# Performance work log

Measured on AMD Instinct MI355X. Metric: run time of the kernel, lower is better.

Reference implementation:

```python
import jax, jax.numpy as jnp
import numpy as np

# Dims from LiftSplatShootGPN defaults
B, N, D, FH, FW, C = 8, 6, 41, 8, 22, 64
OGFH, OGFW = 128, 352
DX = jnp.array([0.5, 0.5, 20.0], dtype=jnp.float32)        # gen_dx_bx
BX = jnp.array([-49.75, -49.75, 0.0], dtype=jnp.float32)
NX = (200, 200, 1)


def _frustum():
    # D x fH x fW x 3, matches create_frustum
    ds = jnp.broadcast_to(jnp.arange(4.0, 45.0, 1.0, dtype=jnp.float32).reshape(D, 1, 1), (D, FH, FW))
    xs = jnp.broadcast_to(jnp.linspace(0.0, OGFW - 1.0, FW, dtype=jnp.float32).reshape(1, 1, FW), (D, FH, FW))
    ys = jnp.broadcast_to(jnp.linspace(0.0, OGFH - 1.0, FH, dtype=jnp.float32).reshape(1, FH, 1), (D, FH, FW))
    return jnp.stack((xs, ys, ds), -1)


def setup_inputs() -> dict:
    key = jax.random.key(0)
    k1, k2, k3, k4, k5, k6 = jax.random.split(key, 6)
    eye = jnp.eye(3, dtype=jnp.float32)
    x_feats = jax.random.normal(k1, (B, N, D, FH, FW, C), dtype=jnp.float32)
    # well-conditioned camera extrinsics / intrinsics
    rots = eye + 0.1 * jax.random.normal(k2, (B, N, 3, 3), dtype=jnp.float32)
    trans = 2.0 * jax.random.normal(k3, (B, N, 3), dtype=jnp.float32)
    intr_base = jnp.array([[278.0, 0.0, 176.0], [0.0, 278.0, 64.0], [0.0, 0.0, 1.0]], dtype=jnp.float32)
    intrins = intr_base + 0.5 * jax.random.normal(k4, (B, N, 3, 3), dtype=jnp.float32) * jnp.array([[1, 0, 1], [0, 1, 1], [0, 0, 0]], dtype=jnp.float32)
    post_rots = eye + 0.01 * jax.random.normal(k5, (B, N, 3, 3), dtype=jnp.float32)
    post_trans = 0.5 * jax.random.normal(k6, (B, N, 3), dtype=jnp.float32)
    return {"x_feats": x_feats, "rots": rots, "trans": trans, "intrins": intrins,
            "post_rots": post_rots, "post_trans": post_trans}


def _forward(x_feats, rots, trans, intrins, post_rots, post_trans):
    frustum = _frustum()  # [D,FH,FW,3]
    # get_geometry: undo image-space augmentation
    pts = frustum[None, None] - post_trans[:, :, None, None, None, :]            # [B,N,D,H,W,3]
    inv_pr = jnp.linalg.inv(post_rots)                                           # [B,N,3,3]
    pts = jnp.einsum('bnij,bndhwj->bndhwi', inv_pr, pts)
    # unproject: (u*d, v*d, d)
    pts = jnp.concatenate((pts[..., :2] * pts[..., 2:3], pts[..., 2:3]), axis=-1)
    combine = jnp.einsum('bnij,bnjk->bnik', rots, jnp.linalg.inv(intrins))
    geom = jnp.einsum('bnij,bndhwj->bndhwi', combine, pts) + trans[:, :, None, None, None, :]

    # voxel_pooling
    Nprime = B * N * D * FH * FW
    x = x_feats.reshape(Nprime, C)
    # torch .long() truncates toward zero -> astype(int32) matches
    g = ((geom - (BX - DX / 2.0)) / DX).reshape(Nprime, 3).astype(jnp.int32)
    bix = jnp.repeat(jnp.arange(B, dtype=jnp.int32), Nprime // B)
    kept = ((g[:, 0] >= 0) & (g[:, 0] < NX[0]) &
            (g[:, 1] >= 0) & (g[:, 1] < NX[1]) &
            (g[:, 2] >= 0) & (g[:, 2] < NX[2]))
    # QuickCumsum computes per-voxel segment sums; scatter-add of all kept points
    # into the dense grid yields identical values without the sort.
    flat = ((bix * NX[2] + g[:, 2]) * NX[0] + g[:, 0]) * NX[1] + g[:, 1]
    flat = jnp.where(kept, flat, 0)
    xm = jnp.where(kept[:, None], x, jnp.zeros((), x.dtype))
    grid = jnp.zeros((B * NX[2] * NX[0] * NX[1], C), dtype=x.dtype).at[flat].add(xm)
    # final: [B, C, nz, nx0, nx1] -> cat over nz (nz=1) -> [B, C, 200, 200]
    grid = grid.reshape(B, NX[2], NX[0], NX[1], C)
    final = jnp.transpose(grid, (0, 1, 4, 2, 3)).reshape(B, NX[2] * C, NX[0], NX[1])
    return final


def reference(x_feats, rots, trans, intrins, post_rots, post_trans):
    return _forward(x_feats, rots, trans, intrins, post_rots, post_trans)
```

## Files before the change

kernel.cpp:

```cpp
#include <hip/hip_runtime.h>

#define B_   8
#define N_   6
#define D_   41
#define FH_  8
#define FW_  22
#define C_   64
#define NPRIME (B_*N_*D_*FH_*FW_)
#define NBLK_PTS 1353
#define PTS_PER_CAM (D_*FH_*FW_)
#define NX0  200
#define NX1  200
#define G1H  2
#define NB2  (B_ * NX0 * G1H)
#define OUTSZ (B_*C_*NX0*NX1)
#define RROWS 4
#define NGRP  50
#define KINT  25
#define NCH   4

__device__ void lapack_inv3_f32(const float Ain[9], float Aout[9]) {
    #pragma clang fp contract(off)
    float a[9];
    for (int r = 0; r < 3; ++r)
        for (int c = 0; c < 3; ++c)
            a[c*3 + r] = Ain[r*3 + c];
    int ipiv[3];
    for (int j = 0; j < 3; ++j) {
        int p = j;
        float amax = fabsf(a[j*3 + j]);
        for (int i = j + 1; i < 3; ++i) {
            float v = fabsf(a[j*3 + i]);
            if (v > amax) { amax = v; p = i; }
        }
        ipiv[j] = p;
        if (p != j)
            for (int c = 0; c < 3; ++c) { float t = a[c*3+j]; a[c*3+j] = a[c*3+p]; a[c*3+p] = t; }
        float d = 1.0f / a[j*3 + j];
        for (int i = j + 1; i < 3; ++i) a[j*3 + i] = a[j*3 + i] * d;
        for (int jj = j + 1; jj < 3; ++jj) {
            float temp = -a[jj*3 + j];
            for (int ii = j + 1; ii < 3; ++ii)
                a[jj*3 + ii] = a[jj*3 + ii] + a[j*3 + ii] * temp;
        }
    }
    for (int j = 0; j < 3; ++j) {
        float ajj_inv = 1.0f / a[j*3 + j];
        a[j*3 + j] = ajj_inv;
        float AJJ = -ajj_inv;
        for (int jj = 0; jj < j; ++jj) {
            float temp = a[j*3 + jj];
            for (int i = 0; i < jj; ++i)
                a[j*3 + i] = a[j*3 + i] + temp * a[jj*3 + i];
            a[j*3 + jj] = a[j*3 + jj] * a[jj*3 + jj];
        }
        for (int i = 0; i < j; ++i) a[j*3 + i] = a[j*3 + i] * AJJ;
    }
    float work[3];
    for (int j = 2; j >= 0; --j) {
        for (int i = j + 1; i < 3; ++i) { work[i] = a[j*3 + i]; a[j*3 + i] = 0.0f; }
        for (int jj = j + 1; jj < 3; ++jj) {
            float temp = -work[jj];
            for (int i = 0; i < 3; ++i)
                a[j*3 + i] = a[j*3 + i] + temp * a[jj*3 + i];
        }
    }
    for (int j = 2; j >= 0; --j) {
        int p = ipiv[j];
        if (p != j)
            for (int i = 0; i < 3; ++i) { float t = a[j*3+i]; a[j*3+i] = a[p*3+i]; a[p*3+i] = t; }
    }
    for (int r = 0; r < 3; ++r)
        for (int c = 0; c < 3; ++c)
            Aout[r*3 + c] = a[c*3 + r];
}

__global__ void prep_kernel(const float* __restrict__ rots,
                            const float* __restrict__ trans,
                            const float* __restrict__ intrins,
                            const float* __restrict__ post_rots,
                            const float* __restrict__ post_trans,
                            float* __restrict__ mats,
                            int* __restrict__ counts) {
    #pragma clang fp contract(off)
    int t = threadIdx.x;
    for (int i = t; i < NB2; i += 256) counts[i] = 0;
    if (t >= B_ * N_) return;
    float pr[9], ipr[9], K[9], iK[9];
    for (int i = 0; i < 9; ++i) { pr[i] = post_rots[t*9 + i]; K[i] = intrins[t*9 + i]; }
    lapack_inv3_f32(pr, ipr);
    lapack_inv3_f32(K, iK);
    float* m = mats + t * 24;
    for (int i = 0; i < 9; ++i) m[i] = ipr[i];
    for (int i = 0; i < 3; ++i)
        for (int k = 0; k < 3; ++k) {
            float s = rots[t*9 + i*3 + 0] * iK[0*3 + k];
            s = s + rots[t*9 + i*3 + 1] * iK[1*3 + k];
            s = s + rots[t*9 + i*3 + 2] * iK[2*3 + k];
            m[9 + i*3 + k] = s;
        }
    for (int i = 0; i < 3; ++i) {
        m[18 + i] = post_trans[t*3 + i];
        m[21 + i] = trans[t*3 + i];
    }
}

__global__ void __launch_bounds__(256) geom_kernel(
        const float* __restrict__ mats,
        unsigned int* __restrict__ pcode,
        int* __restrict__ counts) {
    #pragma clang fp contract(off)
    __shared__ unsigned int hist[NB2];
    int t = threadIdx.x;
    int p = blockIdx.x * 256 + t;
    for (int i = t; i < NB2; i += 256) hist[i] = 0u;
    __syncthreads();

    int w  = p % FW_;
    int h  = (p / FW_) % FH_;
    int d  = (p / (FW_ * FH_)) % D_;
    int bn = p / PTS_PER_CAM;
    int b  = bn / N_;

    const float* m = mats + bn * 24;

    float xs = (w == FW_ - 1) ? 351.0f : (float)((double)w * (351.0 / 21.0));
    float ys = (h == FH_ - 1) ? 127.0f : (float)((double)h * (127.0 / 7.0));
    float ds = 4.0f + (float)d;

    float px = xs - m[18], py = ys - m[19], pz = ds - m[20];
    float qx = m[0]*px;  qx = qx + m[1]*py;  qx = qx + m[2]*pz;
    float qy = m[3]*px;  qy = qy + m[4]*py;  qy = qy + m[5]*pz;
    float qz = m[6]*px;  qz = qz + m[7]*py;  qz = qz + m[8]*pz;

    float ux = qx * qz, uy = qy * qz, uz = qz;

    float gx = m[9]*ux;   gx = gx + m[10]*uy;  gx = gx + m[11]*uz;  gx = gx + m[21];
    float gy = m[12]*ux;  gy = gy + m[13]*uy;  gy = gy + m[14]*uz;  gy = gy + m[22];
    float gz = m[15]*ux;  gz = gz + m[16]*uy;  gz = gz + m[17]*uz;  gz = gz + m[23];

    float cx = (gx - (-50.0f)) / 0.5f;
    float cy = (gy - (-50.0f)) / 0.5f;
    float cz = (gz - (-10.0f)) / 20.0f;
    int g0 = (int)cx;
    int g1 = (int)cy;
    int g2 = (int)cz;

    bool kept = (g0 >= 0) && (g0 < NX0) && (g1 >= 0) && (g1 < NX1) && (g2 == 0);
    if (kept) {
        int g1h = g1 / 100;
        int r   = g1 - g1h * 100;
        int bk  = (b * NX0 + g0) * G1H + g1h;
        pcode[p] = ((unsigned int)bk << 7) | (unsigned int)r;
        atomicAdd(&hist[bk], 1u);
    } else {
        pcode[p] = 0xFFFFFFFFu;
    }
    __syncthreads();
    for (int i = t; i < NB2; i += 256) {
        unsigned int hv = hist[i];
        if (hv) atomicAdd(&counts[i], (int)hv);
    }
}

__global__ void scan_kernel(const int* __restrict__ counts,
                            int* __restrict__ offsets,
                            int* __restrict__ cursor) {
    __shared__ int ts[128];
    int t = threadIdx.x;
    const int PER = NB2 / 128;
    int base = t * PER;
    int mysum = 0;
    for (int j = 0; j < PER; ++j) mysum += counts[base + j];
    ts[t] = mysum;
    __syncthreads();
    for (int off = 1; off < 128; off <<= 1) {
        int v = (t >= off) ? ts[t - off] : 0;
        __syncthreads();
        ts[t] += v;
        __syncthreads();
    }
    int run = (t > 0) ? ts[t - 1] : 0;
    for (int j = 0; j < PER; ++j) {
        offsets[base + j] = run;
        cursor[base + j]  = run;
        run += counts[base + j];
    }
    if (t == 127) offsets[NB2] = run;
}

__global__ void __launch_bounds__(256) place_kernel(
        const unsigned int* __restrict__ pcode,
        int* __restrict__ cursor,
        unsigned int* __restrict__ entries) {
    __shared__ int cnt[NB2];
    int t = threadIdx.x;
    int p = blockIdx.x * 256 + t;
    for (int i = t; i < NB2; i += 256) cnt[i] = 0;
    __syncthreads();
    unsigned int code = pcode[p];
    bool kept = (code != 0xFFFFFFFFu);
    int bk = (int)(code >> 7);
    int lr = 0;
    if (kept) lr = atomicAdd(&cnt[bk], 1);
    __syncthreads();
    for (int i = t; i < NB2; i += 256) {
        int c = cnt[i];
        if (c) cnt[i] = atomicAdd(&cursor[i], c);
    }
    __syncthreads();
    if (kept) {
        int r   = (int)(code & 127u);
        int bh  = bk >> 1;
        int g0  = bh % NX0;
        int g1  = (bk & 1) * 100 + r;
        entries[cnt[bk] + lr] = ((unsigned int)(g0 & 15) << 27) |
                                ((unsigned int)g1 << 19) | (unsigned int)p;
    }
}

__global__ void __launch_bounds__(256) render_kernel(
        const float* __restrict__ x_feats,
        const unsigned int* __restrict__ entries,
        const int* __restrict__ offsets,
        float* __restrict__ out) {
    __shared__ float acc[NCH * RROWS * NX1];
    const int CHS = RROWS * NX1;
    int blk = blockIdx.x;
    int k   = blk % KINT;
    int cg  = (blk / KINT) & 15;
    int b   = blk / (KINT * 16);
    int c0  = cg * NCH;
    int t   = threadIdx.x;

    for (int g = k; g < NGRP; g += KINT) {
        int row0 = g * RROWS;

        for (int i = t; i < NCH * CHS; i += 256) acc[i] = 0.0f;
        __syncthreads();

        int bk0 = b * (NX0 * G1H) + row0 * G1H;
        int s = offsets[bk0];
        int e = offsets[bk0 + RROWS * G1H];
        for (int i = s + t; i < e; i += 256) {
            unsigned int v = entries[i];
            int p  = (int)(v & 0x7FFFFu);
            int g1 = (int)((v >> 19) & 0xFFu);
            int rl = (int)(v >> 27) & 3;
            float4 f = *(const float4*)&x_feats[(size_t)p * C_ + c0];
            int a = rl * NX1 + g1;
            atomicAdd(&acc[a], f.x);
            atomicAdd(&acc[CHS + a], f.y);
            atomicAdd(&acc[2 * CHS + a], f.z);
            atomicAdd(&acc[3 * CHS + a], f.w);
        }
        __syncthreads();

        size_t pl = ((size_t)b * C_ + c0) * (NX0 * NX1) + (size_t)row0 * NX1;
        const int nf4 = CHS / 4;
        for (int k2 = t; k2 < NCH * nf4; k2 += 256) {
            int ch = k2 / nf4, kk = k2 - ch * nf4;
            float4 v4 = *(float4*)&acc[ch * CHS + kk * 4];
            *(float4*)&out[pl + (size_t)ch * (NX0 * NX1) + (size_t)kk * 4] = v4;
        }
        __syncthreads();
    }
}

extern "C" void kernel_launch(void* const* d_in, const int* in_sizes, int n_in,
                              void* d_out, int out_size, void* d_ws, size_t ws_size,
                              hipStream_t stream) {
    const float* x_feats    = (const float*)d_in[0];
    const float* rots       = (const float*)d_in[1];
    const float* trans      = (const float*)d_in[2];
    const float* intrins    = (const float*)d_in[3];
    const float* post_rots  = (const float*)d_in[4];
    const float* post_trans = (const float*)d_in[5];
    float* out = (float*)d_out;

    char* w = (char*)d_ws;
    float*        mats       = (float*)w;         w += 48 * 24 * sizeof(float);
    int*          counts     = (int*)w;           w += NB2 * sizeof(int);
    int*          offsets    = (int*)w;           w += (NB2 + 1) * sizeof(int);
    int*          cursor     = (int*)w;           w += NB2 * sizeof(int);
    unsigned int* pcode      = (unsigned int*)w;  w += NPRIME * sizeof(unsigned int);
    unsigned int* entries    = (unsigned int*)w;  w += NPRIME * sizeof(unsigned int);

    prep_kernel<<<1, 256, 0, stream>>>(rots, trans, intrins, post_rots, post_trans,
                                       mats, counts);
    geom_kernel<<<NBLK_PTS, 256, 0, stream>>>(mats, pcode, counts);
    scan_kernel<<<1, 128, 0, stream>>>(counts, offsets, cursor);
    place_kernel<<<NBLK_PTS, 256, 0, stream>>>(pcode, cursor, entries);
    render_kernel<<<B_ * 16 * KINT, 256, 0, stream>>>(x_feats, entries, offsets, out);
}
```

Measured before the change: 196.2 us.

## Render one BEV row per tile with 16 channels per block

The render kernel now handles one grid row per group and 16 channels per block, where it used to handle four rows and 4 channels. Each entry therefore loads 64 contiguous bytes of features and does 16 shared-memory atomics, so the entry list is scanned 4 times instead of 16. The row-in-group bits are dropped from the packed entry and the shared accumulator is padded to 204 per channel. The trade is fewer blocks (1280 vs 3200), a higher per-thread atomic count and shorter per-row work lists.

```diff
diff --git a/kernel.cpp b/kernel.cpp
--- a/kernel.cpp
+++ b/kernel.cpp
@@ -14,10 +14,10 @@
 #define G1H  2
 #define NB2  (B_ * NX0 * G1H)
 #define OUTSZ (B_*C_*NX0*NX1)
-#define RROWS 4
-#define NGRP  50
-#define KINT  25
-#define NCH   4
+#define NGRP  200
+#define KINT  40
+#define NCH   16
+#define CHS   204
 
 __device__ void lapack_inv3_f32(const float Ain[9], float Aout[9]) {
     #pragma clang fp contract(off)
@@ -211,11 +211,8 @@
     __syncthreads();
     if (kept) {
         int r   = (int)(code & 127u);
-        int bh  = bk >> 1;
-        int g0  = bh % NX0;
         int g1  = (bk & 1) * 100 + r;
-        entries[cnt[bk] + lr] = ((unsigned int)(g0 & 15) << 27) |
-                                ((unsigned int)g1 << 19) | (unsigned int)p;
+        entries[cnt[bk] + lr] = ((unsigned int)g1 << 19) | (unsigned int)p;
     }
 }
 
@@ -224,42 +221,52 @@
         const unsigned int* __restrict__ entries,
         const int* __restrict__ offsets,
         float* __restrict__ out) {
-    __shared__ float acc[NCH * RROWS * NX1];
-    const int CHS = RROWS * NX1;
+    __shared__ float acc[NCH * CHS];
     int blk = blockIdx.x;
     int k   = blk % KINT;
-    int cg  = (blk / KINT) & 15;
-    int b   = blk / (KINT * 16);
+    int cg  = (blk / KINT) & 3;
+    int b   = blk / (KINT * 4);
     int c0  = cg * NCH;
     int t   = threadIdx.x;
 
     for (int g = k; g < NGRP; g += KINT) {
-        int row0 = g * RROWS;
-
         for (int i = t; i < NCH * CHS; i += 256) acc[i] = 0.0f;
         __syncthreads();
 
-        int bk0 = b * (NX0 * G1H) + row0 * G1H;
+        int bk0 = b * (NX0 * G1H) + g * G1H;
         int s = offsets[bk0];
-        int e = offsets[bk0 + RROWS * G1H];
+        int e = offsets[bk0 + G1H];
         for (int i = s + t; i < e; i += 256) {
             unsigned int v = entries[i];
             int p  = (int)(v & 0x7FFFFu);
             int g1 = (int)((v >> 19) & 0xFFu);
-            int rl = (int)(v >> 27) & 3;
-            float4 f = *(const float4*)&x_feats[(size_t)p * C_ + c0];
-            int a = rl * NX1 + g1;
-            atomicAdd(&acc[a], f.x);
-            atomicAdd(&acc[CHS + a], f.y);
-            atomicAdd(&acc[2 * CHS + a], f.z);
-            atomicAdd(&acc[3 * CHS + a], f.w);
-        }
-        __syncthreads();
-
-        size_t pl = ((size_t)b * C_ + c0) * (NX0 * NX1) + (size_t)row0 * NX1;
-        const int nf4 = CHS / 4;
-        for (int k2 = t; k2 < NCH * nf4; k2 += 256) {
-            int ch = k2 / nf4, kk = k2 - ch * nf4;
+            const float4* xp = (const float4*)&x_feats[(size_t)p * C_ + c0];
+            float4 f0 = xp[0];
+            float4 f1 = xp[1];
+            float4 f2 = xp[2];
+            float4 f3 = xp[3];
+            atomicAdd(&acc[ 0 * CHS + g1], f0.x);
+            atomicAdd(&acc[ 1 * CHS + g1], f0.y);
+            atomicAdd(&acc[ 2 * CHS + g1], f0.z);
+            atomicAdd(&acc[ 3 * CHS + g1], f0.w);
+            atomicAdd(&acc[ 4 * CHS + g1], f1.x);
+            atomicAdd(&acc[ 5 * CHS + g1], f1.y);
+            atomicAdd(&acc[ 6 * CHS + g1], f1.z);
+            atomicAdd(&acc[ 7 * CHS + g1], f1.w);
+            atomicAdd(&acc[ 8 * CHS + g1], f2.x);
+            atomicAdd(&acc[ 9 * CHS + g1], f2.y);
+            atomicAdd(&acc[10 * CHS + g1], f2.z);
+            atomicAdd(&acc[11 * CHS + g1], f2.w);
+            atomicAdd(&acc[12 * CHS + g1], f3.x);
+            atomicAdd(&acc[13 * CHS + g1], f3.y);
+            atomicAdd(&acc[14 * CHS + g1], f3.z);
+            atomicAdd(&acc[15 * CHS + g1], f3.w);
+        }
+        __syncthreads();
+
+        size_t pl = ((size_t)b * C_ + c0) * (NX0 * NX1) + (size_t)g * NX1;
+        for (int k2 = t; k2 < NCH * 50; k2 += 256) {
+            int ch = k2 / 50, kk = k2 - ch * 50;
             float4 v4 = *(float4*)&acc[ch * CHS + kk * 4];
             *(float4*)&out[pl + (size_t)ch * (NX0 * NX1) + (size_t)kk * 4] = v4;
         }
@@ -291,5 +298,5 @@
     geom_kernel<<<NBLK_PTS, 256, 0, stream>>>(mats, pcode, counts);
     scan_kernel<<<1, 128, 0, stream>>>(counts, offsets, cursor);
     place_kernel<<<NBLK_PTS, 256, 0, stream>>>(pcode, cursor, entries);
-    render_kernel<<<B_ * 16 * KINT, 256, 0, stream>>>(x_feats, entries, offsets, out);
-}
+    render_kernel<<<B_ * 4 * KINT, 256, 0, stream>>>(x_feats, entries, offsets, out);
+}
```

Result: faster. 188.7 us (-3.9%).
